# Kernel tuning notes

Hardware: AMD Instinct MI355X
Metric: run time of the kernel (lower is better)

Reference implementation:

```python
import jax, jax.numpy as jnp
import numpy as np

T, B, D, L, A, H = 64, 256, 512, 50, 18, 32


def setup_inputs() -> dict:
    key = jax.random.key(0)
    ks = jax.random.split(key, 12)
    s = 0.05
    return {
        "state": jax.random.normal(ks[0], (T, B, D), jnp.float32),
        "demonstration": jax.random.normal(ks[1], (T, B, L, D), jnp.float32),
        "h0": jnp.zeros((1, B, H), jnp.float32),
        "c0": jnp.zeros((1, B, H), jnp.float32),
        # attn: Linear(H + D, L)
        "W_attn": jax.random.normal(ks[2], (L, H + D), jnp.float32) * s,
        "b_attn": jnp.zeros((L,), jnp.float32),
        # attn_combine: Linear(2*D, H)
        "W_comb": jax.random.normal(ks[3], (H, 2 * D), jnp.float32) * s,
        "b_comb": jnp.zeros((H,), jnp.float32),
        # LSTM(H, H): gate order i, f, g, o
        "W_ih": jax.random.normal(ks[4], (4 * H, H), jnp.float32) * s,
        "b_ih": jnp.zeros((4 * H,), jnp.float32),
        "W_hh": jax.random.normal(ks[5], (4 * H, H), jnp.float32) * s,
        "b_hh": jnp.zeros((4 * H,), jnp.float32),
        # middle: Linear(H, 2H); output: Linear(2H, A)
        "W_mid": jax.random.normal(ks[6], (2 * H, H), jnp.float32) * s,
        "b_mid": jnp.zeros((2 * H,), jnp.float32),
        "W_out": jax.random.normal(ks[7], (A, 2 * H), jnp.float32) * s,
        "b_out": jnp.zeros((A,), jnp.float32),
    }


def reference(state, demonstration, h0, c0, W_attn, b_attn, W_comb, b_comb,
              W_ih, b_ih, W_hh, b_hh, W_mid, b_mid, W_out, b_out):
    def step(carry, inp):
        h, c = carry                         # [B,H], [B,H]
        cur, demo = inp                      # [B,D], [B,L,D]
        logits = jnp.concatenate([cur, h], axis=-1) @ W_attn.T + b_attn  # [B,L]
        w = jax.nn.softmax(logits, axis=1)
        applied = jnp.einsum('bl,bld->bd', w, demo)                      # [B,D]
        x = jax.nn.relu(jnp.concatenate([applied, cur], axis=-1) @ W_comb.T + b_comb)  # [B,H]
        gates = x @ W_ih.T + b_ih + h @ W_hh.T + b_hh                    # [B,4H]
        i, f, g, o = jnp.split(gates, 4, axis=-1)
        c_new = jax.nn.sigmoid(f) * c + jax.nn.sigmoid(i) * jnp.tanh(g)
        h_new = jax.nn.sigmoid(o) * jnp.tanh(c_new)
        mid = h_new @ W_mid.T + b_mid                                    # [B,2H]
        q = mid @ W_out.T + b_out                                        # [B,A]
        return (h_new, c_new), q

    (hT, cT), q = jax.lax.scan(step, (h0[0], c0[0]), (state, demonstration))
    return q, hT[None], cT[None]
```

## Files before the change

kernel.cpp:

```cpp
#include <hip/hip_runtime.h>
#include <cstddef>

#define T_ 64
#define B_ 256
#define D_ 512
#define L_ 50
#define A_ 18
#define H_ 32

typedef __attribute__((ext_vector_type(8))) short short8;
typedef __attribute__((ext_vector_type(4))) float f32x4;

constexpr size_t WS_LC = 0;
constexpr size_t WS_CC = 819200;
constexpr size_t WS_DP = 1868416;

__device__ __forceinline__ float sigf(float x) { return 1.f / (1.f + expf(-x)); }

__device__ __forceinline__ short f2bf_rne(float f) {
  unsigned u = __float_as_uint(f);
  return (short)((u + 0x7fffu + ((u >> 16) & 1u)) >> 16);
}
__device__ __forceinline__ float bcast(float v, int l) {
  return __int_as_float(__builtin_amdgcn_readlane(__float_as_int(v), l));
}
__device__ __forceinline__ void glds16(const float* g, float* l) {
  __builtin_amdgcn_global_load_lds((const __attribute__((address_space(1))) unsigned*)g,
                                   (__attribute__((address_space(3))) unsigned*)l, 16, 0, 0);
}
__device__ __forceinline__ void glds4(const float* g, float* l) {
  __builtin_amdgcn_global_load_lds((const __attribute__((address_space(1))) unsigned*)g,
                                   (__attribute__((address_space(3))) unsigned*)l, 4, 0, 0);
}

__global__ __launch_bounds__(256) void precompute3(
    const float* __restrict__ state,
    const float* __restrict__ W_attn, const float* __restrict__ b_attn,
    const float* __restrict__ W_comb, const float* __restrict__ b_comb,
    float* __restrict__ lc, float* __restrict__ cc) {
  extern __shared__ char pm3[];
  float* As = (float*)pm3;
  short* Bf = (short*)(pm3 + 16384);
  const int tid = threadIdx.x;
  const int wave = tid >> 6, lane = tid & 63;
  const int r0 = blockIdx.x * 64;

  const int srow = lane >> 3;
  const int scol = (((lane & 7) * 16) ^ (srow << 4)) >> 2;
  const int crow = lane & 15, g = lane >> 4;
  const int cb0 = (g * 32) ^ ((crow & 7) << 4);

  f32x4 acc[6];
#pragma unroll
  for (int nt = 0; nt < 6; ++nt) acc[nt] = {0.f, 0.f, 0.f, 0.f};

#define STAGE_A(KI, SLOT)                                                       \
  {                                                                             \
    float* dst_ = As + ((SLOT) * 4 + wave) * 512;                               \
    _Pragma("unroll")                                                           \
    for (int i_ = 0; i_ < 2; ++i_) {                                            \
      const float* src_ = state +                                               \
          (size_t)(r0 + wave * 16 + i_ * 8 + srow) * 512 + (KI) * 32 + scol;    \
      glds16(src_, dst_ + i_ * 256);                                            \
    }                                                                           \
  }

  auto stageB = [&](int ko) {
#pragma unroll
    for (int it = 0; it < 6; ++it) {
      int u = tid + it * 256;
      int l = u & 63;
      int nt = (u >> 6) % 6;
      int c = u / 384;
      int n = nt * 16 + (l & 15);
      int kb = ko * 128 + c * 32 + ((l >> 4) << 3);
      f32x4 v0 = {0.f, 0.f, 0.f, 0.f}, v1 = {0.f, 0.f, 0.f, 0.f};
      if (n < 50) {
        const f32x4* s = (const f32x4*)(W_attn + (size_t)n * 544 + kb);
        v0 = s[0]; v1 = s[1];
      } else if (n < 82) {
        const f32x4* s = (const f32x4*)(W_comb + (size_t)(n - 50) * 1024 + 512 + kb);
        v0 = s[0]; v1 = s[1];
      }
      short8 hi, lo;
#pragma unroll
      for (int j = 0; j < 4; ++j) {
        unsigned ua = __float_as_uint(v0[j]), ha = ua & 0xffff0000u;
        hi[j] = (short)(ha >> 16);
        lo[j] = f2bf_rne(v0[j] - __uint_as_float(ha));
        unsigned ub = __float_as_uint(v1[j]), hb = ub & 0xffff0000u;
        hi[4 + j] = (short)(hb >> 16);
        lo[4 + j] = f2bf_rne(v1[j] - __uint_as_float(hb));
      }
      *(short8*)&Bf[(((0 * 4 + c) * 6 + nt) * 64 + l) * 8] = hi;
      *(short8*)&Bf[(((1 * 4 + c) * 6 + nt) * 64 + l) * 8] = lo;
    }
  };

  STAGE_A(0, 0);
  stageB(0);
  asm volatile("s_waitcnt lgkmcnt(0)" ::: "memory");
  __builtin_amdgcn_s_barrier();

  for (int ko = 0; ko < 4; ++ko) {
    if (ko > 0) {
      __builtin_amdgcn_s_barrier();
      stageB(ko);
      asm volatile("s_waitcnt lgkmcnt(0)" ::: "memory");
      __builtin_amdgcn_s_barrier();
    }
#pragma unroll
    for (int c = 0; c < 4; ++c) {
      const int ki = ko * 4 + c;
      if (ki < 15) {
        STAGE_A(ki + 1, (ki + 1) & 1);
        asm volatile("s_waitcnt vmcnt(2)" ::: "memory");
      } else {
        asm volatile("s_waitcnt vmcnt(0)" ::: "memory");
      }
      __builtin_amdgcn_sched_barrier(0);
      const char* ab = (const char*)(As + ((ki & 1) * 4 + wave) * 512) + crow * 128;
      f32x4 a0 = *(const f32x4*)(ab + cb0);
      f32x4 a1 = *(const f32x4*)(ab + (cb0 ^ 16));
      short8 ahi, alo;
#pragma unroll
      for (int j = 0; j < 4; ++j) {
        unsigned ua = __float_as_uint(a0[j]), ha = ua & 0xffff0000u;
        ahi[j] = (short)(ha >> 16);
        alo[j] = f2bf_rne(a0[j] - __uint_as_float(ha));
        unsigned ub = __float_as_uint(a1[j]), hb = ub & 0xffff0000u;
        ahi[4 + j] = (short)(hb >> 16);
        alo[4 + j] = f2bf_rne(a1[j] - __uint_as_float(hb));
      }
#pragma unroll
      for (int nt = 0; nt < 6; ++nt) {
        short8 bh = *(const short8*)&Bf[(((0 * 4 + c) * 6 + nt) * 64 + lane) * 8];
        short8 bl = *(const short8*)&Bf[(((1 * 4 + c) * 6 + nt) * 64 + lane) * 8];
        acc[nt] = __builtin_amdgcn_mfma_f32_16x16x32_bf16(ahi, bh, acc[nt], 0, 0, 0);
        acc[nt] = __builtin_amdgcn_mfma_f32_16x16x32_bf16(alo, bh, acc[nt], 0, 0, 0);
        acc[nt] = __builtin_amdgcn_mfma_f32_16x16x32_bf16(ahi, bl, acc[nt], 0, 0, 0);
      }
    }
  }
#undef STAGE_A

#pragma unroll
  for (int nt = 0; nt < 6; ++nt) {
    const int n = nt * 16 + crow;
    float bias = 0.f;
    if (n < 50) bias = b_attn[n];
    else if (n < 82) bias = b_comb[n - 50];
#pragma unroll
    for (int reg = 0; reg < 4; ++reg) {
      const int r = r0 + wave * 16 + (g << 2) + reg;
      const float vv = acc[nt][reg] + bias;
      if (n < 50) lc[(size_t)r * 50 + n] = vv;
      else if (n < 82) cc[(size_t)r * 32 + (n - 50)] = vv;
    }
  }
}

__global__ __launch_bounds__(512, 2) void dp_gemm(const float* __restrict__ demo,
                                                  const float* __restrict__ W_comb,
                                                  float* __restrict__ dp) {
  extern __shared__ char smraw[];
  float* Abuf = (float*)smraw;
  short* frag = (short*)(smraw + 98304);
  const int tid = threadIdx.x;

  for (int f = tid; f < 16384; f += 512) {
    int j = f & 7, l = (f >> 3) & 63, nt = (f >> 9) & 1, c = f >> 10;
    int n = nt * 16 + (l & 15);
    int k = c * 32 + ((l >> 4) << 3) + j;
    float v = W_comb[(size_t)n * 1024 + k];
    unsigned u = __float_as_uint(v);
    unsigned hb = u & 0xffff0000u;
    frag[(((0 * 16 + c) * 2 + nt) * 64 + l) * 8 + j] = (short)(hb >> 16);
    frag[(((1 * 16 + c) * 2 + nt) * 64 + l) * 8 + j] = f2bf_rne(v - __uint_as_float(hb));
  }
  __syncthreads();

  const int wave = tid >> 6, lane = tid & 63;
  const size_t row0 = (size_t)blockIdx.x * 3200;

  int rrl[4], gcol[4];
#pragma unroll
  for (int i = 0; i < 4; ++i) {
    rrl[i] = wave * 16 + i * 4 + (lane >> 4);
    gcol[i] = ((((lane & 15) * 16) ^ ((rrl[i] & 7) << 4)) >> 2);
  }
  const int rr = wave * 16 + (lane & 15);
  const int g = lane >> 4;

  f32x4 acc0 = {0.f, 0.f, 0.f, 0.f}, acc1 = {0.f, 0.f, 0.f, 0.f};

#define STAGE(Q, SLOT)                                                          \
  {                                                                             \
    const int tile_ = (Q) >> 3, kc_ = (Q) & 7;                                  \
    const size_t rbase_ = row0 + (size_t)tile_ * 128;                           \
    float* dst_ = Abuf + (SLOT) * 8192 + wave * 1024;                           \
    _Pragma("unroll")                                                           \
    for (int i = 0; i < 4; ++i) {                                               \
      const float* src_ = demo + (rbase_ + rrl[i]) * 512 + kc_ * 64 + gcol[i];  \
      glds16(src_, dst_ + i * 256);                                             \
    }                                                                           \
  }

  STAGE(0, 0);
  STAGE(1, 1);
  for (int q = 0; q < 200; ++q) {
    const int q2 = (q + 2 < 200) ? q + 2 : 199;
    STAGE(q2, (q + 2) % 3);
    if (q >= 8 && (q & 7) <= 1) {
      asm volatile("s_waitcnt vmcnt(16)" ::: "memory");
    } else {
      asm volatile("s_waitcnt vmcnt(8)" ::: "memory");
    }
    __builtin_amdgcn_sched_barrier(0);
    if ((q & 7) == 0) {
      acc0 = {0.f, 0.f, 0.f, 0.f};
      acc1 = {0.f, 0.f, 0.f, 0.f};
    }
    const char* ab = (const char*)(Abuf + (q % 3) * 8192) + rr * 256;
#pragma unroll
    for (int sub = 0; sub < 2; ++sub) {
      const int b0 = (sub * 128 + g * 32) ^ ((rr & 7) << 4);
      f32x4 a0 = *(const f32x4*)(ab + b0);
      f32x4 a1 = *(const f32x4*)(ab + (b0 ^ 16));
      short8 ahi, alo;
#pragma unroll
      for (int j = 0; j < 4; ++j) {
        float v = a0[j];
        unsigned u = __float_as_uint(v), hb = u & 0xffff0000u;
        ahi[j] = (short)(hb >> 16);
        alo[j] = f2bf_rne(v - __uint_as_float(hb));
        float w = a1[j];
        unsigned u2 = __float_as_uint(w), hb2 = u2 & 0xffff0000u;
        ahi[4 + j] = (short)(hb2 >> 16);
        alo[4 + j] = f2bf_rne(w - __uint_as_float(hb2));
      }
      const int ck = (q & 7) * 2 + sub;
      short8 bh0 = *(const short8*)&frag[(((0 + ck) * 2 + 0) * 64 + lane) * 8];
      short8 bh1 = *(const short8*)&frag[(((0 + ck) * 2 + 1) * 64 + lane) * 8];
      short8 bl0 = *(const short8*)&frag[(((16 + ck) * 2 + 0) * 64 + lane) * 8];
      short8 bl1 = *(const short8*)&frag[(((16 + ck) * 2 + 1) * 64 + lane) * 8];
      acc0 = __builtin_amdgcn_mfma_f32_16x16x32_bf16(ahi, bh0, acc0, 0, 0, 0);
      acc1 = __builtin_amdgcn_mfma_f32_16x16x32_bf16(ahi, bh1, acc1, 0, 0, 0);
      acc0 = __builtin_amdgcn_mfma_f32_16x16x32_bf16(alo, bh0, acc0, 0, 0, 0);
      acc1 = __builtin_amdgcn_mfma_f32_16x16x32_bf16(alo, bh1, acc1, 0, 0, 0);
      acc0 = __builtin_amdgcn_mfma_f32_16x16x32_bf16(ahi, bl0, acc0, 0, 0, 0);
      acc1 = __builtin_amdgcn_mfma_f32_16x16x32_bf16(ahi, bl1, acc1, 0, 0, 0);
    }
    if ((q & 7) == 7) {
      float* drow = dp + (row0 + (size_t)(q >> 3) * 128 + wave * 16) * 32;
#pragma unroll
      for (int reg = 0; reg < 4; ++reg) {
        int r = ((lane >> 4) << 2) + reg;
        drow[r * 32 + (lane & 15)] = acc0[reg];
        drow[r * 32 + 16 + (lane & 15)] = acc1[reg];
      }
    }
  }
#undef STAGE
}

__global__ __launch_bounds__(64, 1) void seq3(
    const float* __restrict__ h0, const float* __restrict__ c0,
    const float* __restrict__ W_attn,
    const float* __restrict__ W_ih, const float* __restrict__ b_ih,
    const float* __restrict__ W_hh, const float* __restrict__ b_hh,
    const float* __restrict__ W_mid, const float* __restrict__ b_mid,
    const float* __restrict__ W_out, const float* __restrict__ b_out,
    const float* __restrict__ ws, float* __restrict__ out) {
  __shared__ alignas(16) float dpb[3][1600];
  __shared__ alignas(16) float lcb[3][64];
  __shared__ alignas(16) float ccb[3][64];
  __shared__ alignas(16) float hist[T_ * 33];
  __shared__ float swq[576];
  __shared__ float sbq[20];
  const int b = blockIdx.x, lane = threadIdx.x, hh = lane & 31;
  const float* lcg = ws + WS_LC;
  const float* ccg = ws + WS_CC;
  const float* dpg = ws + WS_DP;

  float wA2[32], wia[32], wib[32], wha[32], whb[32];
  const int l_eff = lane < 50 ? lane : 49;
#pragma unroll
  for (int k = 0; k < 32; ++k) {
    wA2[k] = W_attn[(size_t)l_eff * 544 + 512 + k];
    wia[k] = W_ih[lane * 32 + k];
    wib[k] = W_ih[(64 + lane) * 32 + k];
    wha[k] = W_hh[lane * 32 + k];
    whb[k] = W_hh[(64 + lane) * 32 + k];
  }
  const float bga = b_ih[lane] + b_hh[lane];
  const float bgb = b_ih[64 + lane] + b_hh[64 + lane];
  float h = h0[b * 32 + hh], c = c0[b * 32 + hh];

#pragma unroll
  for (int tt = 0; tt < 2; ++tt) {
    const size_t rown = (size_t)tt * B_ + b;
    const float* dsrc = dpg + rown * 1600;
#pragma unroll
    for (int i = 0; i < 6; ++i) glds16(dsrc + i * 256 + lane * 4, &dpb[tt][i * 256]);
    glds4(dsrc + 1536 + lane, &dpb[tt][1536]);
    glds4(lcg + rown * 50 + lane, &lcb[tt][0]);
    glds4(ccg + rown * 32 + lane, &ccb[tt][0]);
  }

  for (int idx = lane; idx < 576; idx += 64) {
    int a = idx >> 5, k = idx & 31;
    float acc = 0.f;
#pragma unroll
    for (int m = 0; m < 64; ++m) acc = fmaf(W_out[a * 64 + m], W_mid[m * 32 + k], acc);
    swq[k * 18 + a] = acc;
  }
  if (lane < 18) {
    float acc = b_out[lane];
#pragma unroll
    for (int m = 0; m < 64; ++m) acc = fmaf(W_out[lane * 64 + m], b_mid[m], acc);
    sbq[lane] = acc;
  }

  int p = 0;
  for (int t = 0; t < T_; ++t) {
    const int pn = (p >= 1) ? p - 1 : p + 2;
    {
      const size_t rown = (size_t)(t + 2) * B_ + b;
      const float* dsrc = dpg + rown * 1600;
#pragma unroll
      for (int i = 0; i < 6; ++i) glds16(dsrc + i * 256 + lane * 4, &dpb[pn][i * 256]);
      glds4(dsrc + 1536 + lane, &dpb[pn][1536]);
      glds4(lcg + rown * 50 + lane, &lcb[pn][0]);
      glds4(ccg + rown * 32 + lane, &ccb[pn][0]);
    }
    asm volatile("s_waitcnt vmcnt(18)" ::: "memory");
    __builtin_amdgcn_sched_barrier(0);

    float lg0 = 0.f, lg1 = 0.f;
#pragma unroll
    for (int k = 0; k < 32; k += 2) {
      lg0 = fmaf(bcast(h, k), wA2[k], lg0);
      lg1 = fmaf(bcast(h, k + 1), wA2[k + 1], lg1);
    }
    const float logit = (lane < 50) ? (lcb[p][lane] + lg0 + lg1) : -1e30f;
    float mx = logit;
#pragma unroll
    for (int off = 32; off; off >>= 1) mx = fmaxf(mx, __shfl_xor(mx, off, 64));
    const float e = (lane < 50) ? expf(logit - mx) : 0.f;
    float se = e;
#pragma unroll
    for (int off = 32; off; off >>= 1) se += __shfl_xor(se, off, 64);
    const float wsm = e / se;

    float xl0 = 0.f, xl1 = 0.f;
#pragma unroll
    for (int l = 0; l < 50; l += 2) {
      xl0 = fmaf(bcast(wsm, l), dpb[p][l * 32 + hh], xl0);
      xl1 = fmaf(bcast(wsm, l + 1), dpb[p][(l + 1) * 32 + hh], xl1);
    }
    const float x = fmaxf(xl0 + xl1 + ccb[p][hh], 0.f);

    float ga0 = bga, ga1 = 0.f, gb0 = bgb, gb1 = 0.f;
#pragma unroll
    for (int k = 0; k < 32; k += 2) {
      float xv0 = bcast(x, k), hv0 = bcast(h, k);
      float xv1 = bcast(x, k + 1), hv1 = bcast(h, k + 1);
      ga0 = fmaf(xv0, wia[k], ga0);     ga0 = fmaf(hv0, wha[k], ga0);
      ga1 = fmaf(xv1, wia[k + 1], ga1); ga1 = fmaf(hv1, wha[k + 1], ga1);
      gb0 = fmaf(xv0, wib[k], gb0);     gb0 = fmaf(hv0, whb[k], gb0);
      gb1 = fmaf(xv1, wib[k + 1], gb1); gb1 = fmaf(hv1, whb[k + 1], gb1);
    }
    const float ga = ga0 + ga1, gb = gb0 + gb1;
    const float xga = __shfl_xor(ga, 32, 64), xgb = __shfl_xor(gb, 32, 64);
    const bool low = lane < 32;
    const float iv = low ? ga : xga, fv = low ? xga : ga;
    const float gv = low ? gb : xgb, ov = low ? xgb : gb;
    c = sigf(fv) * c + sigf(iv) * tanhf(gv);
    h = sigf(ov) * tanhf(c);
    if (lane < 32) hist[t * 33 + hh] = h;

    p = (p + 1 == 3) ? 0 : p + 1;
  }

  for (int idx = lane; idx < T_ * A_; idx += 64) {
    int t = idx / A_, a = idx - t * A_;
    float acc = sbq[a];
#pragma unroll
    for (int k = 0; k < 32; ++k) acc = fmaf(hist[t * 33 + k], swq[k * 18 + a], acc);
    out[((size_t)t * B_ + b) * A_ + a] = acc;
  }
  if (lane < 32) {
    out[(size_t)T_ * B_ * A_ + (size_t)b * H_ + lane] = h;
    out[(size_t)T_ * B_ * A_ + (size_t)B_ * H_ + (size_t)b * H_ + lane] = c;
  }
}

extern "C" void kernel_launch(void* const* d_in, const int* in_sizes, int n_in,
                              void* d_out, int out_size, void* d_ws, size_t ws_size,
                              hipStream_t stream) {
  const float* state  = (const float*)d_in[0];
  const float* demo   = (const float*)d_in[1];
  const float* h0     = (const float*)d_in[2];
  const float* c0     = (const float*)d_in[3];
  const float* W_attn = (const float*)d_in[4];
  const float* b_attn = (const float*)d_in[5];
  const float* W_comb = (const float*)d_in[6];
  const float* b_comb = (const float*)d_in[7];
  const float* W_ih   = (const float*)d_in[8];
  const float* b_ih   = (const float*)d_in[9];
  const float* W_hh   = (const float*)d_in[10];
  const float* b_hh   = (const float*)d_in[11];
  const float* W_mid  = (const float*)d_in[12];
  const float* b_mid  = (const float*)d_in[13];
  const float* W_out  = (const float*)d_in[14];
  const float* b_out  = (const float*)d_in[15];
  float* out = (float*)d_out;
  float* ws  = (float*)d_ws;

  constexpr int pm3_smem = 65536;
  (void)hipFuncSetAttribute(reinterpret_cast<const void*>(precompute3),
                            hipFuncAttributeMaxDynamicSharedMemorySize, pm3_smem);
  precompute3<<<dim3(256), dim3(256), pm3_smem, stream>>>(
      state, W_attn, b_attn, W_comb, b_comb, ws + WS_LC, ws + WS_CC);

  constexpr int dp_smem = 163840;
  (void)hipFuncSetAttribute(reinterpret_cast<const void*>(dp_gemm),
                            hipFuncAttributeMaxDynamicSharedMemorySize, dp_smem);
  dp_gemm<<<dim3(256), dim3(512), dp_smem, stream>>>(demo, W_comb, ws + WS_DP);

  seq3<<<dim3(256), dim3(64), 0, stream>>>(
      h0, c0, W_attn, W_ih, b_ih, W_hh, b_hh,
      W_mid, b_mid, W_out, b_out, ws, out);
}
```

Measured before the change: 550.4 us.

## Replace LDS-staged dp GEMM with direct global loads and more smaller blocks

```diff
diff --git a/kernel.cpp b/kernel.cpp
--- a/kernel.cpp
+++ b/kernel.cpp
@@ -160,15 +160,14 @@
   }
 }
 
-__global__ __launch_bounds__(512, 2) void dp_gemm(const float* __restrict__ demo,
-                                                  const float* __restrict__ W_comb,
-                                                  float* __restrict__ dp) {
+__global__ __launch_bounds__(256, 2) void dp_gemm2(const float* __restrict__ demo,
+                                                   const float* __restrict__ W_comb,
+                                                   float* __restrict__ dp) {
   extern __shared__ char smraw[];
-  float* Abuf = (float*)smraw;
-  short* frag = (short*)(smraw + 98304);
+  short* frag = (short*)smraw;
   const int tid = threadIdx.x;
 
-  for (int f = tid; f < 16384; f += 512) {
+  for (int f = tid; f < 16384; f += 256) {
     int j = f & 7, l = (f >> 3) & 63, nt = (f >> 9) & 1, c = f >> 10;
     int n = nt * 16 + (l & 15);
     int k = c * 32 + ((l >> 4) << 3) + j;
@@ -181,69 +180,31 @@
   __syncthreads();
 
   const int wave = tid >> 6, lane = tid & 63;
-  const size_t row0 = (size_t)blockIdx.x * 3200;
-
-  int rrl[4], gcol[4];
-#pragma unroll
-  for (int i = 0; i < 4; ++i) {
-    rrl[i] = wave * 16 + i * 4 + (lane >> 4);
-    gcol[i] = ((((lane & 15) * 16) ^ ((rrl[i] & 7) << 4)) >> 2);
-  }
-  const int rr = wave * 16 + (lane & 15);
-  const int g = lane >> 4;
-
-  f32x4 acc0 = {0.f, 0.f, 0.f, 0.f}, acc1 = {0.f, 0.f, 0.f, 0.f};
-
-#define STAGE(Q, SLOT)                                                          \
-  {                                                                             \
-    const int tile_ = (Q) >> 3, kc_ = (Q) & 7;                                  \
-    const size_t rbase_ = row0 + (size_t)tile_ * 128;                           \
-    float* dst_ = Abuf + (SLOT) * 8192 + wave * 1024;                           \
-    _Pragma("unroll")                                                           \
-    for (int i = 0; i < 4; ++i) {                                               \
-      const float* src_ = demo + (rbase_ + rrl[i]) * 512 + kc_ * 64 + gcol[i];  \
-      glds16(src_, dst_ + i * 256);                                             \
-    }                                                                           \
-  }
-
-  STAGE(0, 0);
-  STAGE(1, 1);
-  for (int q = 0; q < 200; ++q) {
-    const int q2 = (q + 2 < 200) ? q + 2 : 199;
-    STAGE(q2, (q + 2) % 3);
-    if (q >= 8 && (q & 7) <= 1) {
-      asm volatile("s_waitcnt vmcnt(16)" ::: "memory");
-    } else {
-      asm volatile("s_waitcnt vmcnt(8)" ::: "memory");
-    }
-    __builtin_amdgcn_sched_barrier(0);
-    if ((q & 7) == 0) {
-      acc0 = {0.f, 0.f, 0.f, 0.f};
-      acc1 = {0.f, 0.f, 0.f, 0.f};
-    }
-    const char* ab = (const char*)(Abuf + (q % 3) * 8192) + rr * 256;
-#pragma unroll
-    for (int sub = 0; sub < 2; ++sub) {
-      const int b0 = (sub * 128 + g * 32) ^ ((rr & 7) << 4);
-      f32x4 a0 = *(const f32x4*)(ab + b0);
-      f32x4 a1 = *(const f32x4*)(ab + (b0 ^ 16));
+  const int r = lane & 15, g = lane >> 4;
+  const size_t row0 = (size_t)blockIdx.x * 1600 + wave * 16;
+
+  for (int tile = 0; tile < 25; ++tile) {
+    const size_t rbase = row0 + (size_t)tile * 64;
+    const float* arow = demo + (rbase + r) * 512 + g * 8;
+    f32x4 acc0 = {0.f, 0.f, 0.f, 0.f}, acc1 = {0.f, 0.f, 0.f, 0.f};
+#pragma unroll
+    for (int kc = 0; kc < 16; ++kc) {
+      f32x4 a0 = *(const f32x4*)(arow + kc * 32);
+      f32x4 a1 = *(const f32x4*)(arow + kc * 32 + 4);
       short8 ahi, alo;
 #pragma unroll
       for (int j = 0; j < 4; ++j) {
-        float v = a0[j];
-        unsigned u = __float_as_uint(v), hb = u & 0xffff0000u;
+        unsigned u = __float_as_uint(a0[j]), hb = u & 0xffff0000u;
         ahi[j] = (short)(hb >> 16);
-        alo[j] = f2bf_rne(v - __uint_as_float(hb));
-        float w = a1[j];
-        unsigned u2 = __float_as_uint(w), hb2 = u2 & 0xffff0000u;
+        alo[j] = f2bf_rne(a0[j] - __uint_as_float(hb));
+        unsigned u2 = __float_as_uint(a1[j]), hb2 = u2 & 0xffff0000u;
         ahi[4 + j] = (short)(hb2 >> 16);
-        alo[4 + j] = f2bf_rne(w - __uint_as_float(hb2));
-      }
-      const int ck = (q & 7) * 2 + sub;
-      short8 bh0 = *(const short8*)&frag[(((0 + ck) * 2 + 0) * 64 + lane) * 8];
-      short8 bh1 = *(const short8*)&frag[(((0 + ck) * 2 + 1) * 64 + lane) * 8];
-      short8 bl0 = *(const short8*)&frag[(((16 + ck) * 2 + 0) * 64 + lane) * 8];
-      short8 bl1 = *(const short8*)&frag[(((16 + ck) * 2 + 1) * 64 + lane) * 8];
+        alo[4 + j] = f2bf_rne(a1[j] - __uint_as_float(hb2));
+      }
+      short8 bh0 = *(const short8*)&frag[(((0 * 16 + kc) * 2 + 0) * 64 + lane) * 8];
+      short8 bh1 = *(const short8*)&frag[(((0 * 16 + kc) * 2 + 1) * 64 + lane) * 8];
+      short8 bl0 = *(const short8*)&frag[(((1 * 16 + kc) * 2 + 0) * 64 + lane) * 8];
+      short8 bl1 = *(const short8*)&frag[(((1 * 16 + kc) * 2 + 1) * 64 + lane) * 8];
       acc0 = __builtin_amdgcn_mfma_f32_16x16x32_bf16(ahi, bh0, acc0, 0, 0, 0);
       acc1 = __builtin_amdgcn_mfma_f32_16x16x32_bf16(ahi, bh1, acc1, 0, 0, 0);
       acc0 = __builtin_amdgcn_mfma_f32_16x16x32_bf16(alo, bh0, acc0, 0, 0, 0);
@@ -251,17 +212,14 @@
       acc0 = __builtin_amdgcn_mfma_f32_16x16x32_bf16(ahi, bl0, acc0, 0, 0, 0);
       acc1 = __builtin_amdgcn_mfma_f32_16x16x32_bf16(ahi, bl1, acc1, 0, 0, 0);
     }
-    if ((q & 7) == 7) {
-      float* drow = dp + (row0 + (size_t)(q >> 3) * 128 + wave * 16) * 32;
-#pragma unroll
-      for (int reg = 0; reg < 4; ++reg) {
-        int r = ((lane >> 4) << 2) + reg;
-        drow[r * 32 + (lane & 15)] = acc0[reg];
-        drow[r * 32 + 16 + (lane & 15)] = acc1[reg];
-      }
-    }
-  }
-#undef STAGE
+    float* drow = dp + rbase * 32;
+#pragma unroll
+    for (int reg = 0; reg < 4; ++reg) {
+      const int rw = (g << 2) + reg;
+      drow[rw * 32 + r] = acc0[reg];
+      drow[rw * 32 + 16 + r] = acc1[reg];
+    }
+  }
 }
 
 __global__ __launch_bounds__(64, 1) void seq3(
@@ -424,10 +382,10 @@
   precompute3<<<dim3(256), dim3(256), pm3_smem, stream>>>(
       state, W_attn, b_attn, W_comb, b_comb, ws + WS_LC, ws + WS_CC);
 
-  constexpr int dp_smem = 163840;
-  (void)hipFuncSetAttribute(reinterpret_cast<const void*>(dp_gemm),
-                            hipFuncAttributeMaxDynamicSharedMemorySize, dp_smem);
-  dp_gemm<<<dim3(256), dim3(512), dp_smem, stream>>>(demo, W_comb, ws + WS_DP);
+  constexpr int dp2_smem = 65536;
+  (void)hipFuncSetAttribute(reinterpret_cast<const void*>(dp_gemm2),
+                            hipFuncAttributeMaxDynamicSharedMemorySize, dp2_smem);
+  dp_gemm2<<<dim3(512), dim3(256), dp2_smem, stream>>>(demo, W_comb, ws + WS_DP);
 
   seq3<<<dim3(256), dim3(64), 0, stream>>>(
       h0, c0, W_attn, W_ih, b_ih, W_hh, b_hh,
```

After: 634.1 us. 15.2% more time.
